# Kernel optimization log

Measured on AMD Instinct MI355X. Metric: run time of the kernel, lower is better.

The kernel has to match this reference:

```python
import jax, jax.numpy as jnp
import numpy as np

N_NODES = 100000
N_EDGES = 3200000
D_IN = 256
D_OUT = 256


def setup_inputs() -> dict:
    key = jax.random.key(0)
    k1, k2, k3, k4, k5 = jax.random.split(key, 5)
    x = jax.random.normal(k1, (N_NODES, D_IN), dtype=jnp.float32)
    edge_row = jax.random.randint(k2, (N_EDGES,), 0, N_NODES, dtype=jnp.int32)
    edge_col = jax.random.randint(k3, (N_EDGES,), 0, N_NODES, dtype=jnp.int32)
    edge_val = jax.random.uniform(k4, (N_EDGES,), dtype=jnp.float32)
    # Linear weight [out_dim, in_dim], kaiming-uniform-like scale
    bound = 1.0 / np.sqrt(D_IN)
    W = jax.random.uniform(k5, (D_OUT, D_IN), dtype=jnp.float32,
                           minval=-bound, maxval=bound)
    return {"x": x, "edge_row": edge_row, "edge_col": edge_col,
            "edge_val": edge_val, "W": W}


def reference(x, edge_row, edge_col, edge_val, W):
    # SpMM: agg[i] = sum_{edges e with row=i} val_e * x[col_e]
    msgs = edge_val[:, None] * x[edge_col]            # [E, D_IN] gather
    agg = jax.ops.segment_sum(msgs, edge_row, num_segments=N_NODES)  # [N, D_IN]
    # Dense linear projection (bias=False): agg @ W.T
    return agg @ W.T                                  # [N, D_OUT]
```

## Files before the change

kernel.cpp:

```cpp
#include <hip/hip_runtime.h>
#include <stdint.h>

#define N_NODES 100000
#define N_EDGES 3200000
#define D_FEAT 256
#define CHUNK 8192
#define NBLK_E 391
#define NBKT 391
#define CT 1024

typedef __attribute__((ext_vector_type(8))) short short8;
typedef __attribute__((ext_vector_type(8))) ushort ushort8;
typedef __attribute__((ext_vector_type(4))) float float4v;

__device__ inline unsigned short f2bf(float f) {
    union { float f; unsigned u; } v; v.f = f;
    unsigned u = v.u;
    u += 0x7FFF + ((u >> 16) & 1);
    return (unsigned short)(u >> 16);
}
__device__ inline float bf2f(unsigned short u) {
    union { unsigned u; float f; } v; v.u = (unsigned)u << 16;
    return v.f;
}

__global__ void wconv_kernel(const float* __restrict__ W, ushort* __restrict__ Wbf) {
    int i = blockIdx.x * 256 + threadIdx.x;
    Wbf[i] = f2bf(W[i]);
}

__global__ __launch_bounds__(256) void gemm_x_kernel(
        const float* __restrict__ x,
        const ushort* __restrict__ Wbf,
        ushort* __restrict__ ybf) {
    int w    = threadIdx.x >> 6;
    int lane = threadIdx.x & 63;
    int quad = lane >> 4;
    int l16  = lane & 15;
    int rt   = blockIdx.x * 64;

    float4v acc[4][4];
    #pragma unroll
    for (int mt = 0; mt < 4; ++mt)
        #pragma unroll
        for (int nt = 0; nt < 4; ++nt) acc[mt][nt] = (float4v){0.f, 0.f, 0.f, 0.f};

    #pragma unroll
    for (int k0 = 0; k0 < 256; k0 += 32) {
        short8 a[4], bf[4];
        #pragma unroll
        for (int mt = 0; mt < 4; ++mt) {
            int row = rt + mt * 16 + l16;
            if (row >= N_NODES) row = N_NODES - 1;
            const float4v* p = (const float4v*)&x[(size_t)row * 256 + k0 + quad * 8];
            float4v f0 = p[0], f1 = p[1];
            a[mt][0] = (short)f2bf(f0.x); a[mt][1] = (short)f2bf(f0.y);
            a[mt][2] = (short)f2bf(f0.z); a[mt][3] = (short)f2bf(f0.w);
            a[mt][4] = (short)f2bf(f1.x); a[mt][5] = (short)f2bf(f1.y);
            a[mt][6] = (short)f2bf(f1.z); a[mt][7] = (short)f2bf(f1.w);
        }
        #pragma unroll
        for (int nt = 0; nt < 4; ++nt) {
            int n = w * 64 + nt * 16 + l16;
            bf[nt] = *(const short8*)&Wbf[n * 256 + k0 + quad * 8];
        }
        #pragma unroll
        for (int mt = 0; mt < 4; ++mt)
            #pragma unroll
            for (int nt = 0; nt < 4; ++nt)
                acc[mt][nt] = __builtin_amdgcn_mfma_f32_16x16x32_bf16(a[mt], bf[nt], acc[mt][nt], 0, 0, 0);
    }
    #pragma unroll
    for (int mt = 0; mt < 4; ++mt)
        #pragma unroll
        for (int nt = 0; nt < 4; ++nt) {
            int n = w * 64 + nt * 16 + l16;
            #pragma unroll
            for (int r = 0; r < 4; ++r) {
                int row = rt + mt * 16 + quad * 4 + r;
                if (row < N_NODES) ybf[(size_t)row * 256 + n] = f2bf(acc[mt][nt][r]);
            }
        }
}

__global__ __launch_bounds__(CT) void hist_kernel(const int* __restrict__ erow,
                                                  int* __restrict__ hist) {
    __shared__ int cnt[NBKT];
    if (threadIdx.x < NBKT) cnt[threadIdx.x] = 0;
    __syncthreads();
    int cb = blockIdx.x * CHUNK;
    #pragma unroll
    for (int j = 0; j < CHUNK; j += CT) {
        int i = cb + j + threadIdx.x;
        if (i < N_EDGES) atomicAdd(&cnt[erow[i] >> 8], 1);
    }
    __syncthreads();
    if (threadIdx.x < NBKT) hist[blockIdx.x * NBKT + threadIdx.x] = cnt[threadIdx.x];
}

__global__ __launch_bounds__(512) void scan_blocks(int* __restrict__ hist,
                                                   int* __restrict__ totals) {
    __shared__ int s[512];
    int b = blockIdx.x;
    int t = threadIdx.x;
    int v = (t < NBLK_E) ? hist[t * NBKT + b] : 0;
    s[t] = v;
    __syncthreads();
    for (int o = 1; o < 512; o <<= 1) {
        int x = (t >= o) ? s[t - o] : 0;
        __syncthreads();
        s[t] += x;
        __syncthreads();
    }
    if (t < NBLK_E) hist[t * NBKT + b] = s[t] - v;
    if (t == NBLK_E - 1) totals[b] = s[t];
}

__global__ __launch_bounds__(512) void scan_buckets(const int* __restrict__ totals,
                                                    int* __restrict__ base_,
                                                    int* __restrict__ row_start) {
    __shared__ int s[512];
    int t = threadIdx.x;
    int v = (t < NBKT) ? totals[t] : 0;
    s[t] = v;
    __syncthreads();
    for (int o = 1; o < 512; o <<= 1) {
        int x = (t >= o) ? s[t - o] : 0;
        __syncthreads();
        s[t] += x;
        __syncthreads();
    }
    if (t < NBKT) base_[t] = s[t] - v;
    if (t == 0) { base_[NBKT] = N_EDGES; row_start[N_NODES] = N_EDGES; }
}

__global__ __launch_bounds__(CT) void scatter_kernel(
        const int* __restrict__ erow, const int* __restrict__ ecol,
        const float* __restrict__ eval,
        const int* __restrict__ hist, const int* __restrict__ base_,
        uint2* __restrict__ tmp) {
    __shared__ int lbase[NBKT];
    __shared__ int cnt[NBKT];
    int t = threadIdx.x;
    if (t < NBKT) {
        lbase[t] = hist[blockIdx.x * NBKT + t] + base_[t];
        cnt[t] = 0;
    }
    __syncthreads();
    int cb = blockIdx.x * CHUNK;
    #pragma unroll
    for (int j = 0; j < CHUNK; j += CT) {
        int i = cb + j + t;
        if (i < N_EDGES) {
            int r = erow[i];
            int b = r >> 8;
            int pos = lbase[b] + atomicAdd(&cnt[b], 1);
            uint2 cv;
            cv.x = (unsigned)ecol[i] | ((unsigned)(r & 255) << 17);
            union { float f; unsigned u; } w; w.f = eval[i];
            cv.y = w.u;
            tmp[pos] = cv;
        }
    }
}

__global__ __launch_bounds__(512) void fine_sort(const uint2* __restrict__ tmp,
                                                 const int* __restrict__ base_,
                                                 uint2* __restrict__ csr,
                                                 int* __restrict__ row_start) {
    __shared__ int cnt[256];
    __shared__ int excl[256];
    int b = blockIdx.x;
    int t = threadIdx.x;
    int s0 = base_[b];
    int nb = base_[b + 1] - s0;
    if (t < 256) cnt[t] = 0;
    __syncthreads();
    for (int j = t; j < nb; j += 512)
        atomicAdd(&cnt[tmp[s0 + j].x >> 17], 1);
    __syncthreads();
    int v = 0;
    if (t < 256) { v = cnt[t]; excl[t] = v; }
    __syncthreads();
    for (int o = 1; o < 256; o <<= 1) {
        int x = 0;
        if (t >= o && t < 256) x = excl[t - o];
        __syncthreads();
        if (t < 256) excl[t] += x;
        __syncthreads();
    }
    if (t < 256) {
        int ex = excl[t] - v;
        int row = b * 256 + t;
        if (row < N_NODES) row_start[row] = s0 + ex;
        excl[t] = ex;
        cnt[t] = 0;
    }
    __syncthreads();
    for (int j = t; j < nb; j += 512) {
        uint2 cv = tmp[s0 + j];
        unsigned rl = cv.x >> 17;
        int dst = s0 + excl[rl] + atomicAdd(&cnt[rl], 1);
        csr[dst] = cv;
    }
}

__global__ __launch_bounds__(256) void spmm_kernel(
        const ushort* __restrict__ ybf,
        const int* __restrict__ row_start,
        const uint2* __restrict__ csr_cv,
        float* __restrict__ out) {
    int row  = (blockIdx.x * blockDim.x + threadIdx.x) >> 6;
    int lane = threadIdx.x & 63;
    int half = lane >> 5;
    int hl   = lane & 31;
    if (row >= N_NODES) return;
    int start = row_start[row];
    int end   = row_start[row + 1];
    float acc[8] = {0.f, 0.f, 0.f, 0.f, 0.f, 0.f, 0.f, 0.f};
    int e = start + half;
    for (; e + 6 < end; e += 8) {
        uint2 cv0 = csr_cv[e];
        uint2 cv1 = csr_cv[e + 2];
        uint2 cv2 = csr_cv[e + 4];
        uint2 cv3 = csr_cv[e + 6];
        ushort8 v0 = *(const ushort8*)&ybf[(size_t)(cv0.x & 0x1FFFF) * 256 + hl * 8];
        ushort8 v1 = *(const ushort8*)&ybf[(size_t)(cv1.x & 0x1FFFF) * 256 + hl * 8];
        ushort8 v2 = *(const ushort8*)&ybf[(size_t)(cv2.x & 0x1FFFF) * 256 + hl * 8];
        ushort8 v3 = *(const ushort8*)&ybf[(size_t)(cv3.x & 0x1FFFF) * 256 + hl * 8];
        union { unsigned u; float f; } w0, w1, w2, w3;
        w0.u = cv0.y; w1.u = cv1.y; w2.u = cv2.y; w3.u = cv3.y;
        #pragma unroll
        for (int j = 0; j < 8; ++j) acc[j] += w0.f * bf2f(v0[j]);
        #pragma unroll
        for (int j = 0; j < 8; ++j) acc[j] += w1.f * bf2f(v1[j]);
        #pragma unroll
        for (int j = 0; j < 8; ++j) acc[j] += w2.f * bf2f(v2[j]);
        #pragma unroll
        for (int j = 0; j < 8; ++j) acc[j] += w3.f * bf2f(v3[j]);
    }
    for (; e < end; e += 2) {
        uint2 cv = csr_cv[e];
        ushort8 v = *(const ushort8*)&ybf[(size_t)(cv.x & 0x1FFFF) * 256 + hl * 8];
        union { unsigned u; float f; } w; w.u = cv.y;
        #pragma unroll
        for (int j = 0; j < 8; ++j) acc[j] += w.f * bf2f(v[j]);
    }
    #pragma unroll
    for (int j = 0; j < 8; ++j) acc[j] += __shfl_xor(acc[j], 32, 64);
    if (half == 0) {
        float4v o0 = {acc[0], acc[1], acc[2], acc[3]};
        float4v o1 = {acc[4], acc[5], acc[6], acc[7]};
        *(float4v*)&out[(size_t)row * 256 + hl * 8]     = o0;
        *(float4v*)&out[(size_t)row * 256 + hl * 8 + 4] = o1;
    }
}


extern "C" void kernel_launch(void* const* d_in, const int* in_sizes, int n_in,
                              void* d_out, int out_size, void* d_ws, size_t ws_size,
                              hipStream_t stream) {
    const float* x    = (const float*)d_in[0];
    const int*   erow = (const int*)d_in[1];
    const int*   ecol = (const int*)d_in[2];
    const float* eval = (const float*)d_in[3];
    const float* W    = (const float*)d_in[4];
    float* out = (float*)d_out;

    char* ws = (char*)d_ws;
    size_t off = 0;
    int* hist      = (int*)(ws + off);   off += ((size_t)NBLK_E * NBKT * 4 + 255) & ~255ull;
    int* totals    = (int*)(ws + off);   off += (512 * 4);
    int* base_     = (int*)(ws + off);   off += ((size_t)(NBKT + 1) * 4 + 255) & ~255ull;
    int* row_start = (int*)(ws + off);   off += ((size_t)(N_NODES + 1) * 4 + 255) & ~255ull;
    uint2* tmp     = (uint2*)(ws + off); off += (size_t)N_EDGES * 8;
    uint2* csr     = (uint2*)(ws + off); off += (size_t)N_EDGES * 8;
    ushort* Wbf    = (ushort*)(ws + off); off += (size_t)D_FEAT * D_FEAT * 2;
    ushort* ybf    = (ushort*)(ws + off); off += (size_t)N_NODES * D_FEAT * 2;

    wconv_kernel<<<(D_FEAT * D_FEAT) / 256, 256, 0, stream>>>(W, Wbf);
    gemm_x_kernel<<<(N_NODES + 63) / 64, 256, 0, stream>>>(x, Wbf, ybf);

    hist_kernel<<<NBLK_E, CT, 0, stream>>>(erow, hist);
    scan_blocks<<<NBKT, 512, 0, stream>>>(hist, totals);
    scan_buckets<<<1, 512, 0, stream>>>(totals, base_, row_start);
    scatter_kernel<<<NBLK_E, CT, 0, stream>>>(erow, ecol, eval, hist, base_, tmp);
    fine_sort<<<NBKT, 512, 0, stream>>>(tmp, base_, csr, row_start);

    spmm_kernel<<<N_NODES / 4, 256, 0, stream>>>(ybf, row_start, csr, out);
}
```

Baseline: 570.2 us.

## Fuse histogram into GEMM, use atomic bucket cursors, fuse fine sort into SpMM

The coarse row-bucket histogram now runs inside the GEMM kernel, which accumulates global bucket totals with atomics. The per-block scan kernel is dropped, and the scatter kernel claims bucket ranges through atomic cursors, so edge order within a bucket becomes nondeterministic. The fine sort and the SpMM are merged into one kernel per 256-row bucket. Each block sorts its edges into LDS (capacity 9216) and each half-wave processes 16 rows, with a slow fallback scan over global memory if a bucket overflows. This removes several launches and the second global CSR write/read, at the cost of less SpMM parallelism (391 blocks of 512 threads).

```diff
diff --git a/kernel.cpp b/kernel.cpp
--- a/kernel.cpp
+++ b/kernel.cpp
@@ -7,7 +7,8 @@
 #define CHUNK 8192
 #define NBLK_E 391
 #define NBKT 391
-#define CT 1024
+#define EPB 2048
+#define CAP 9216
 
 typedef __attribute__((ext_vector_type(8))) short short8;
 typedef __attribute__((ext_vector_type(8))) ushort ushort8;
@@ -24,15 +25,34 @@
     return v.f;
 }
 
-__global__ void wconv_kernel(const float* __restrict__ W, ushort* __restrict__ Wbf) {
-    int i = blockIdx.x * 256 + threadIdx.x;
-    Wbf[i] = f2bf(W[i]);
+__global__ __launch_bounds__(256) void prep_kernel(const float* __restrict__ W,
+                                                   ushort* __restrict__ Wbf,
+                                                   int* __restrict__ tot) {
+    int b = blockIdx.x;
+    if (b < 256) {
+        int i = b * 256 + threadIdx.x;
+        Wbf[i] = f2bf(W[i]);
+    } else {
+        for (int i = threadIdx.x; i < NBKT; i += 256) tot[i] = 0;
+    }
 }
 
 __global__ __launch_bounds__(256) void gemm_x_kernel(
         const float* __restrict__ x,
         const ushort* __restrict__ Wbf,
+        const int* __restrict__ erow,
+        int* __restrict__ tot,
         ushort* __restrict__ ybf) {
+    __shared__ int hcnt[NBKT];
+    for (int b = threadIdx.x; b < NBKT; b += 256) hcnt[b] = 0;
+    __syncthreads();
+    int eb = blockIdx.x * EPB;
+    #pragma unroll
+    for (int j = 0; j < EPB; j += 256) {
+        int i = eb + j + threadIdx.x;
+        if (i < N_EDGES) atomicAdd(&hcnt[erow[i] >> 8], 1);
+    }
+
     int w    = threadIdx.x >> 6;
     int lane = threadIdx.x & 63;
     int quad = lane >> 4;
@@ -81,29 +101,18 @@
                 if (row < N_NODES) ybf[(size_t)row * 256 + n] = f2bf(acc[mt][nt][r]);
             }
         }
-}
-
-__global__ __launch_bounds__(CT) void hist_kernel(const int* __restrict__ erow,
-                                                  int* __restrict__ hist) {
-    __shared__ int cnt[NBKT];
-    if (threadIdx.x < NBKT) cnt[threadIdx.x] = 0;
-    __syncthreads();
-    int cb = blockIdx.x * CHUNK;
-    #pragma unroll
-    for (int j = 0; j < CHUNK; j += CT) {
-        int i = cb + j + threadIdx.x;
-        if (i < N_EDGES) atomicAdd(&cnt[erow[i] >> 8], 1);
-    }
-    __syncthreads();
-    if (threadIdx.x < NBKT) hist[blockIdx.x * NBKT + threadIdx.x] = cnt[threadIdx.x];
-}
-
-__global__ __launch_bounds__(512) void scan_blocks(int* __restrict__ hist,
-                                                   int* __restrict__ totals) {
+
+    __syncthreads();
+    for (int b = threadIdx.x; b < NBKT; b += 256)
+        if (hcnt[b]) atomicAdd(&tot[b], hcnt[b]);
+}
+
+__global__ __launch_bounds__(512) void scan_buckets(const int* __restrict__ tot,
+                                                    int* __restrict__ base_,
+                                                    int* __restrict__ cur) {
     __shared__ int s[512];
-    int b = blockIdx.x;
     int t = threadIdx.x;
-    int v = (t < NBLK_E) ? hist[t * NBKT + b] : 0;
+    int v = (t < NBKT) ? tot[t] : 0;
     s[t] = v;
     __syncthreads();
     for (int o = 1; o < 512; o <<= 1) {
@@ -112,49 +121,41 @@
         s[t] += x;
         __syncthreads();
     }
-    if (t < NBLK_E) hist[t * NBKT + b] = s[t] - v;
-    if (t == NBLK_E - 1) totals[b] = s[t];
-}
-
-__global__ __launch_bounds__(512) void scan_buckets(const int* __restrict__ totals,
-                                                    int* __restrict__ base_,
-                                                    int* __restrict__ row_start) {
-    __shared__ int s[512];
-    int t = threadIdx.x;
-    int v = (t < NBKT) ? totals[t] : 0;
-    s[t] = v;
-    __syncthreads();
-    for (int o = 1; o < 512; o <<= 1) {
-        int x = (t >= o) ? s[t - o] : 0;
-        __syncthreads();
-        s[t] += x;
-        __syncthreads();
-    }
-    if (t < NBKT) base_[t] = s[t] - v;
-    if (t == 0) { base_[NBKT] = N_EDGES; row_start[N_NODES] = N_EDGES; }
-}
-
-__global__ __launch_bounds__(CT) void scatter_kernel(
+    if (t < NBKT) {
+        base_[t] = s[t] - v;
+        cur[t * 16] = s[t] - v;
+    }
+    if (t == 0) base_[NBKT] = N_EDGES;
+}
+
+__global__ __launch_bounds__(1024) void scatter_kernel(
         const int* __restrict__ erow, const int* __restrict__ ecol,
         const float* __restrict__ eval,
-        const int* __restrict__ hist, const int* __restrict__ base_,
-        uint2* __restrict__ tmp) {
-    __shared__ int lbase[NBKT];
+        int* __restrict__ cur, uint2* __restrict__ tmp) {
     __shared__ int cnt[NBKT];
+    __shared__ int runb[NBKT];
     int t = threadIdx.x;
-    if (t < NBKT) {
-        lbase[t] = hist[blockIdx.x * NBKT + t] + base_[t];
-        cnt[t] = 0;
-    }
+    if (t < NBKT) cnt[t] = 0;
     __syncthreads();
     int cb = blockIdx.x * CHUNK;
     #pragma unroll
-    for (int j = 0; j < CHUNK; j += CT) {
+    for (int j = 0; j < CHUNK; j += 1024) {
+        int i = cb + j + t;
+        if (i < N_EDGES) atomicAdd(&cnt[erow[i] >> 8], 1);
+    }
+    __syncthreads();
+    if (t < NBKT)
+        runb[t] = cnt[t] ? atomicAdd(&cur[t * 16], cnt[t]) : 0;
+    __syncthreads();
+    if (t < NBKT) cnt[t] = 0;
+    __syncthreads();
+    #pragma unroll
+    for (int j = 0; j < CHUNK; j += 1024) {
         int i = cb + j + t;
         if (i < N_EDGES) {
             int r = erow[i];
             int b = r >> 8;
-            int pos = lbase[b] + atomicAdd(&cnt[b], 1);
+            int pos = runb[b] + atomicAdd(&cnt[b], 1);
             uint2 cv;
             cv.x = (unsigned)ecol[i] | ((unsigned)(r & 255) << 17);
             union { float f; unsigned u; } w; w.f = eval[i];
@@ -164,91 +165,93 @@
     }
 }
 
-__global__ __launch_bounds__(512) void fine_sort(const uint2* __restrict__ tmp,
-                                                 const int* __restrict__ base_,
-                                                 uint2* __restrict__ csr,
-                                                 int* __restrict__ row_start) {
+__global__ __launch_bounds__(512) void spmm_bin_kernel(
+        const ushort* __restrict__ ybf,
+        const int* __restrict__ base_,
+        const uint2* __restrict__ tmp,
+        float* __restrict__ out) {
     __shared__ int cnt[256];
-    __shared__ int excl[256];
+    __shared__ int rbase[256];
+    __shared__ uint2 ed[CAP];
+    int t = threadIdx.x;
     int b = blockIdx.x;
-    int t = threadIdx.x;
     int s0 = base_[b];
-    int nb = base_[b + 1] - s0;
+    int s1 = base_[b + 1];
+    int nb = s1 - s0;
+    int nbc = nb < CAP ? nb : CAP;
+
     if (t < 256) cnt[t] = 0;
     __syncthreads();
-    for (int j = t; j < nb; j += 512)
+    for (int j = t; j < nbc; j += 512)
         atomicAdd(&cnt[tmp[s0 + j].x >> 17], 1);
     __syncthreads();
     int v = 0;
-    if (t < 256) { v = cnt[t]; excl[t] = v; }
+    if (t < 256) { v = cnt[t]; rbase[t] = v; }
     __syncthreads();
     for (int o = 1; o < 256; o <<= 1) {
         int x = 0;
-        if (t >= o && t < 256) x = excl[t - o];
-        __syncthreads();
-        if (t < 256) excl[t] += x;
-        __syncthreads();
-    }
-    if (t < 256) {
-        int ex = excl[t] - v;
-        int row = b * 256 + t;
-        if (row < N_NODES) row_start[row] = s0 + ex;
-        excl[t] = ex;
-        cnt[t] = 0;
-    }
-    __syncthreads();
-    for (int j = t; j < nb; j += 512) {
+        if (t >= o && t < 256) x = rbase[t - o];
+        __syncthreads();
+        if (t < 256) rbase[t] += x;
+        __syncthreads();
+    }
+    if (t < 256) { rbase[t] -= v; cnt[t] = 0; }
+    __syncthreads();
+    for (int j = t; j < nbc; j += 512) {
         uint2 cv = tmp[s0 + j];
         unsigned rl = cv.x >> 17;
-        int dst = s0 + excl[rl] + atomicAdd(&cnt[rl], 1);
-        csr[dst] = cv;
-    }
-}
-
-__global__ __launch_bounds__(256) void spmm_kernel(
-        const ushort* __restrict__ ybf,
-        const int* __restrict__ row_start,
-        const uint2* __restrict__ csr_cv,
-        float* __restrict__ out) {
-    int row  = (blockIdx.x * blockDim.x + threadIdx.x) >> 6;
-    int lane = threadIdx.x & 63;
+        ed[rbase[rl] + atomicAdd(&cnt[rl], 1)] = cv;
+    }
+    __syncthreads();
+
+    int wave = t >> 6;
+    int lane = t & 63;
     int half = lane >> 5;
     int hl   = lane & 31;
-    if (row >= N_NODES) return;
-    int start = row_start[row];
-    int end   = row_start[row + 1];
-    float acc[8] = {0.f, 0.f, 0.f, 0.f, 0.f, 0.f, 0.f, 0.f};
-    int e = start + half;
-    for (; e + 6 < end; e += 8) {
-        uint2 cv0 = csr_cv[e];
-        uint2 cv1 = csr_cv[e + 2];
-        uint2 cv2 = csr_cv[e + 4];
-        uint2 cv3 = csr_cv[e + 6];
-        ushort8 v0 = *(const ushort8*)&ybf[(size_t)(cv0.x & 0x1FFFF) * 256 + hl * 8];
-        ushort8 v1 = *(const ushort8*)&ybf[(size_t)(cv1.x & 0x1FFFF) * 256 + hl * 8];
-        ushort8 v2 = *(const ushort8*)&ybf[(size_t)(cv2.x & 0x1FFFF) * 256 + hl * 8];
-        ushort8 v3 = *(const ushort8*)&ybf[(size_t)(cv3.x & 0x1FFFF) * 256 + hl * 8];
-        union { unsigned u; float f; } w0, w1, w2, w3;
-        w0.u = cv0.y; w1.u = cv1.y; w2.u = cv2.y; w3.u = cv3.y;
-        #pragma unroll
-        for (int j = 0; j < 8; ++j) acc[j] += w0.f * bf2f(v0[j]);
-        #pragma unroll
-        for (int j = 0; j < 8; ++j) acc[j] += w1.f * bf2f(v1[j]);
-        #pragma unroll
-        for (int j = 0; j < 8; ++j) acc[j] += w2.f * bf2f(v2[j]);
-        #pragma unroll
-        for (int j = 0; j < 8; ++j) acc[j] += w3.f * bf2f(v3[j]);
-    }
-    for (; e < end; e += 2) {
-        uint2 cv = csr_cv[e];
-        ushort8 v = *(const ushort8*)&ybf[(size_t)(cv.x & 0x1FFFF) * 256 + hl * 8];
-        union { unsigned u; float f; } w; w.u = cv.y;
-        #pragma unroll
-        for (int j = 0; j < 8; ++j) acc[j] += w.f * bf2f(v[j]);
-    }
-    #pragma unroll
-    for (int j = 0; j < 8; ++j) acc[j] += __shfl_xor(acc[j], 32, 64);
-    if (half == 0) {
+    int unit = wave * 2 + half;
+    for (int rr = 0; rr < 16; ++rr) {
+        int rl  = unit * 16 + rr;
+        int row = b * 256 + rl;
+        if (row >= N_NODES) continue;
+        int st = rbase[rl];
+        int en = st + cnt[rl];
+        float acc[8] = {0.f, 0.f, 0.f, 0.f, 0.f, 0.f, 0.f, 0.f};
+        int e = st;
+        for (; e + 3 < en; e += 4) {
+            uint2 c0 = ed[e], c1 = ed[e + 1], c2 = ed[e + 2], c3 = ed[e + 3];
+            ushort8 y0 = *(const ushort8*)&ybf[(size_t)(c0.x & 0x1FFFF) * 256 + hl * 8];
+            ushort8 y1 = *(const ushort8*)&ybf[(size_t)(c1.x & 0x1FFFF) * 256 + hl * 8];
+            ushort8 y2 = *(const ushort8*)&ybf[(size_t)(c2.x & 0x1FFFF) * 256 + hl * 8];
+            ushort8 y3 = *(const ushort8*)&ybf[(size_t)(c3.x & 0x1FFFF) * 256 + hl * 8];
+            union { unsigned u; float f; } w0, w1, w2, w3;
+            w0.u = c0.y; w1.u = c1.y; w2.u = c2.y; w3.u = c3.y;
+            #pragma unroll
+            for (int j = 0; j < 8; ++j) acc[j] += w0.f * bf2f(y0[j]);
+            #pragma unroll
+            for (int j = 0; j < 8; ++j) acc[j] += w1.f * bf2f(y1[j]);
+            #pragma unroll
+            for (int j = 0; j < 8; ++j) acc[j] += w2.f * bf2f(y2[j]);
+            #pragma unroll
+            for (int j = 0; j < 8; ++j) acc[j] += w3.f * bf2f(y3[j]);
+        }
+        for (; e < en; ++e) {
+            uint2 c = ed[e];
+            ushort8 y = *(const ushort8*)&ybf[(size_t)(c.x & 0x1FFFF) * 256 + hl * 8];
+            union { unsigned u; float f; } w; w.u = c.y;
+            #pragma unroll
+            for (int j = 0; j < 8; ++j) acc[j] += w.f * bf2f(y[j]);
+        }
+        if (nb > nbc) {
+            for (int j = s0 + nbc; j < s1; ++j) {
+                uint2 c = tmp[j];
+                if ((int)(c.x >> 17) == rl) {
+                    ushort8 y = *(const ushort8*)&ybf[(size_t)(c.x & 0x1FFFF) * 256 + hl * 8];
+                    union { unsigned u; float f; } w; w.u = c.y;
+                    #pragma unroll
+                    for (int j2 = 0; j2 < 8; ++j2) acc[j2] += w.f * bf2f(y[j2]);
+                }
+            }
+        }
         float4v o0 = {acc[0], acc[1], acc[2], acc[3]};
         float4v o1 = {acc[4], acc[5], acc[6], acc[7]};
         *(float4v*)&out[(size_t)row * 256 + hl * 8]     = o0;
@@ -269,23 +272,16 @@
 
     char* ws = (char*)d_ws;
     size_t off = 0;
-    int* hist      = (int*)(ws + off);   off += ((size_t)NBLK_E * NBKT * 4 + 255) & ~255ull;
-    int* totals    = (int*)(ws + off);   off += (512 * 4);
-    int* base_     = (int*)(ws + off);   off += ((size_t)(NBKT + 1) * 4 + 255) & ~255ull;
-    int* row_start = (int*)(ws + off);   off += ((size_t)(N_NODES + 1) * 4 + 255) & ~255ull;
-    uint2* tmp     = (uint2*)(ws + off); off += (size_t)N_EDGES * 8;
-    uint2* csr     = (uint2*)(ws + off); off += (size_t)N_EDGES * 8;
-    ushort* Wbf    = (ushort*)(ws + off); off += (size_t)D_FEAT * D_FEAT * 2;
-    ushort* ybf    = (ushort*)(ws + off); off += (size_t)N_NODES * D_FEAT * 2;
-
-    wconv_kernel<<<(D_FEAT * D_FEAT) / 256, 256, 0, stream>>>(W, Wbf);
-    gemm_x_kernel<<<(N_NODES + 63) / 64, 256, 0, stream>>>(x, Wbf, ybf);
-
-    hist_kernel<<<NBLK_E, CT, 0, stream>>>(erow, hist);
-    scan_blocks<<<NBKT, 512, 0, stream>>>(hist, totals);
-    scan_buckets<<<1, 512, 0, stream>>>(totals, base_, row_start);
-    scatter_kernel<<<NBLK_E, CT, 0, stream>>>(erow, ecol, eval, hist, base_, tmp);
-    fine_sort<<<NBKT, 512, 0, stream>>>(tmp, base_, csr, row_start);
-
-    spmm_kernel<<<N_NODES / 4, 256, 0, stream>>>(ybf, row_start, csr, out);
-}
+    int* tot    = (int*)(ws + off);    off += (512 * 4);
+    int* base_  = (int*)(ws + off);    off += (512 * 4);
+    int* cur    = (int*)(ws + off);    off += ((size_t)NBKT * 16 * 4 + 255) & ~255ull;
+    uint2* tmp  = (uint2*)(ws + off);  off += (size_t)N_EDGES * 8;
+    ushort* Wbf = (ushort*)(ws + off); off += (size_t)D_FEAT * D_FEAT * 2;
+    ushort* ybf = (ushort*)(ws + off); off += (size_t)N_NODES * D_FEAT * 2;
+
+    prep_kernel<<<257, 256, 0, stream>>>(W, Wbf, tot);
+    gemm_x_kernel<<<(N_NODES + 63) / 64, 256, 0, stream>>>(x, Wbf, erow, tot, ybf);
+    scan_buckets<<<1, 512, 0, stream>>>(tot, base_, cur);
+    scatter_kernel<<<NBLK_E, 1024, 0, stream>>>(erow, ecol, eval, cur, tmp);
+    spmm_bin_kernel<<<NBKT, 512, 0, stream>>>(ybf, base_, tmp, out);
+}
```

After: 571.6 us. No clear change (+0.3%).
